# Kernel tuning notes

Measured on AMD Instinct MI355X. Metric: run time of the kernel, lower is better.

## Reference

```python
import jax, jax.numpy as jnp
import numpy as np

S, XD, C, R = 6, 3, 8, 64   # num_freqs, x_dim, num_channels, res_scale
N = 262144
STD = 0.001


def setup_inputs() -> dict:
    key = jax.random.key(0)
    k1, k2, k3 = jax.random.split(key, 3)
    x = jax.random.uniform(k1, (N, XD), dtype=jnp.float32)
    features = jax.random.normal(k2, (S, 2 * XD, C, R, R), dtype=jnp.float32) * STD
    features_2d = jax.random.normal(k3, (S, 2 * XD, C, R, R), dtype=jnp.float32) * STD
    return {"x": x, "features": features, "features_2d": features_2d}


def _bilinear(img, gx, gy):
    # img: [C,H,W]; gx,gy: [P] normalized coords in [-1,1]
    # bilinear grid_sample, align_corners=True, clamped (border) indices
    _, H, W = img.shape
    ix = (gx + 1.0) * 0.5 * (W - 1)
    iy = (gy + 1.0) * 0.5 * (H - 1)
    ix0f = jnp.floor(ix)
    iy0f = jnp.floor(iy)
    wx = ix - ix0f
    wy = iy - iy0f
    ix0 = jnp.clip(ix0f.astype(jnp.int32), 0, W - 1)
    iy0 = jnp.clip(iy0f.astype(jnp.int32), 0, H - 1)
    ix1 = jnp.clip(ix0 + 1, 0, W - 1)
    iy1 = jnp.clip(iy0 + 1, 0, H - 1)
    v00 = img[:, iy0, ix0]  # [C,P]
    v01 = img[:, iy0, ix1]
    v10 = img[:, iy1, ix0]
    v11 = img[:, iy1, ix1]
    return (v00 * (1 - wx) * (1 - wy) + v01 * wx * (1 - wy)
            + v10 * (1 - wx) * wy + v11 * wx * wy)


def reference(x, features, features_2d):
    n = x.shape[0]
    scales = 2.0 ** jnp.arange(S, dtype=x.dtype)                   # [S]
    xb = x[:, None, :] * scales[:, None]                           # [N,S,3]
    latent = jnp.sin(jnp.stack([xb, xb + 0.5 * jnp.pi], axis=-2))  # [N,S,2,3]

    B = S * 2 * XD  # 36 independent (scale, sin/cos, dim) lookups

    # 1D (line) lookup: grid x-coord fixed at 0, y-coord = encoded value
    gy = jnp.transpose(latent.reshape(n, S, 2 * XD), (1, 2, 0)).reshape(B, n)
    gx = jnp.zeros_like(gy)
    fs = jax.vmap(_bilinear)(features.reshape(B, C, R, R), gx, gy)  # [B,C,N]
    fs = fs.reshape(S, 2, XD, C, n)

    # 2D (plane) lookup with cyclic dim pairs (1,2),(2,0),(0,1)
    pairs = jnp.array([[1, 2], [2, 0], [0, 1]])
    g2 = latent[..., pairs]                                        # [N,S,2,3,2]
    gx2 = jnp.transpose(g2[..., 0], (1, 2, 3, 0)).reshape(B, n)
    gy2 = jnp.transpose(g2[..., 1], (1, 2, 3, 0)).reshape(B, n)
    fs2 = jax.vmap(_bilinear)(features_2d.reshape(B, C, R, R), gx2, gy2)
    fs2 = fs2.reshape(S, 2, XD, C, n)

    out = jnp.transpose(fs * fs2, (4, 3, 0, 1, 2))                 # [N,C,S,2,3]
    out = out + latent[:, None]                                    # + PE, broadcast over C
    return out.reshape(n, C * S * 2 * XD)                          # [N, 288]
```

## Files before the change

### kernel.cpp

```cpp
#include <hip/hip_runtime.h>

#define NS 6
#define NXD 3
#define NC 8
#define NR 64
#define NB 36
#define NPOINTS 262144
#define OUTD 288
#define PTS 32

__device__ __forceinline__ unsigned short f2bf(float f) {
    unsigned u = __float_as_uint(f);
    unsigned r = u + 0x7fffu + ((u >> 16) & 1u);
    return (unsigned short)(r >> 16);
}
__device__ __forceinline__ unsigned pack2(float a, float b) {
    return (unsigned)f2bf(a) | ((unsigned)f2bf(b) << 16);
}

#define QSCALE 8192.0f
#define QINV   (1.0f / 8192.0f)

__device__ __forceinline__ unsigned f2q8(float f) {
    float q = rintf(f * QSCALE);
    q = fminf(fmaxf(q, -127.0f), 127.0f);
    return (unsigned)((int)q) & 0xffu;
}

__global__ void build_pxq(const float* __restrict__ F2, unsigned* __restrict__ px) {
    int tid = blockIdx.x * 256 + threadIdx.x;
    const int total = NB * 64 * 64 * NC;
    if (tid >= total) return;
    int c  = tid & 7;
    int xx = (tid >> 3) & 63;
    int y  = (tid >> 9) & 63;
    int b  = tid >> 15;
    const float* img = F2 + (size_t)(b * NC + c) * (NR * NR);
    int x1 = xx < 63 ? xx + 1 : 63;
    int y1 = y  < 63 ? y  + 1 : 63;
    unsigned q00 = f2q8(img[y  * NR + xx]);
    unsigned q01 = f2q8(img[y  * NR + x1]);
    unsigned q10 = f2q8(img[y1 * NR + xx]);
    unsigned q11 = f2q8(img[y1 * NR + x1]);
    px[tid] = q00 | (q01 << 8) | (q10 << 16) | (q11 << 24);
}

__global__ void build_f1q(const float* __restrict__ F, unsigned* __restrict__ f1q) {
    int tid = blockIdx.x * 256 + threadIdx.x;
    const int total = NB * 64 * NC;
    if (tid >= total) return;
    int c = tid & 7;
    int y = (tid >> 3) & 63;
    int b = tid >> 9;
    const float* img = F + (size_t)(b * NC + c) * NR * NR;
    const float sc = 0.5f * QINV;
    float a = sc * (img[y * NR + 31] + img[y * NR + 32]);
    int y1 = y < 63 ? y + 1 : 63;
    float bb = sc * (img[y1 * NR + 31] + img[y1 * NR + 32]);
    f1q[tid] = pack2(a, bb);
}

__global__ __launch_bounds__(256, 4) void encode_kernel(
    const float* __restrict__ x,
    const unsigned* __restrict__ px,
    const unsigned* __restrict__ f1q,
    float* __restrict__ out)
{
    __shared__ float stage[PTS * 289];
    const int t = threadIdx.x;
    const int c = t & 7;
    const int u = t >> 3;
    const int n = blockIdx.x * PTS + u;

    const float xv0 = x[3 * n + 0];
    const float xv1 = x[3 * n + 1];
    const float xv2 = x[3 * n + 2];

    float* stg = &stage[u * 289];

    #pragma unroll
    for (int g = 0; g < 12; ++g) {
        const int s = g >> 1;
        const int p = g & 1;
        const float sc = (float)(1 << s);
        float l0, l1, l2;
        if (p == 0) {
            l0 = __sinf(xv0 * sc); l1 = __sinf(xv1 * sc); l2 = __sinf(xv2 * sc);
        } else {
            l0 = __cosf(xv0 * sc); l1 = __cosf(xv1 * sc); l2 = __cosf(xv2 * sc);
        }
        const int b0 = g * 3;
        #pragma unroll
        for (int k = 0; k < 3; ++k) {
            const int b = b0 + k;
            float gy1 = (k == 0) ? l0 : (k == 1) ? l1 : l2;
            float ga  = (k == 0) ? l1 : (k == 1) ? l2 : l0;
            float gb  = (k == 0) ? l2 : (k == 1) ? l0 : l1;

            float fy = fminf(fmaxf(__builtin_fmaf(gy1, 31.5f, 31.5f), 0.0f), 63.0f);
            float fy0 = floorf(fy);
            float wy = fy - fy0;
            int y0 = (int)fy0;
            unsigned pr = f1q[(b * 64 + y0) * 8 + c];
            float a0 = __uint_as_float(pr << 16);
            float a1 = __uint_as_float(pr & 0xffff0000u);
            float fsv = __builtin_fmaf(a1 - a0, wy, a0);

            float fx2 = fminf(fmaxf(__builtin_fmaf(ga, 31.5f, 31.5f), 0.0f), 63.0f);
            float fy2 = fminf(fmaxf(__builtin_fmaf(gb, 31.5f, 31.5f), 0.0f), 63.0f);
            float fx20 = floorf(fx2);
            float fy20 = floorf(fy2);
            float wx2 = fx2 - fx20;
            float wy2 = fy2 - fy20;
            int xx = (int)fx20;
            int yy = (int)fy20;
            unsigned w = px[((b * 64 + yy) * 64 + xx) * 8 + c];
            float v00 = (float)((int)(w << 24) >> 24);
            float v01 = (float)((int)(w << 16) >> 24);
            float v10 = (float)((int)(w <<  8) >> 24);
            float v11 = (float)((int)w        >> 24);
            float tp = __builtin_fmaf(v01 - v00, wx2, v00);
            float bt = __builtin_fmaf(v11 - v10, wx2, v10);
            float fs2v = __builtin_fmaf(bt - tp, wy2, tp);

            stg[c * 36 + b] = __builtin_fmaf(fsv, fs2v, gy1);
        }
    }
    __syncthreads();

    float* ob = out + (size_t)blockIdx.x * (PTS * OUTD);
    #pragma unroll
    for (int r = 0; r < 36; ++r) {
        int e = t + r * 256;
        int uu = e / 288;
        int v = e - uu * 288;
        ob[e] = stage[uu * 289 + v];
    }
}

extern "C" void kernel_launch(void* const* d_in, const int* in_sizes, int n_in,
                              void* d_out, int out_size, void* d_ws, size_t ws_size,
                              hipStream_t stream)
{
    const float* x  = (const float*)d_in[0];
    const float* F  = (const float*)d_in[1];
    const float* F2 = (const float*)d_in[2];
    float* out = (float*)d_out;

    unsigned* px  = (unsigned*)d_ws;
    unsigned* f1q = px + NB * 64 * 64 * NC;

    build_pxq<<<(NB * 64 * 64 * NC + 255) / 256, 256, 0, stream>>>(F2, px);
    build_f1q<<<(NB * 64 * NC + 255) / 256, 256, 0, stream>>>(F, f1q);
    encode_kernel<<<NPOINTS / PTS, 256, 0, stream>>>(x, px, f1q, out);
}
```

Before: 371.4 us.

## Split work per thread across scale halves and two channels with uint2 gathers

Reassigns each thread from one channel across all 36 lookups to two adjacent channels across half the scales (18 lookups). Table reads become 8-byte uint2 gathers, and the sin/cos and index math is shared between the two channels, halving transcendental and address work per output. The upper clamp to 63 is dropped because sin/cos outputs stay within range. The risk is more register pressure and a different bank pattern on the shared-memory stage writes.

```diff
diff --git a/kernel.cpp b/kernel.cpp
--- a/kernel.cpp
+++ b/kernel.cpp
@@ -67,63 +67,82 @@
     float* __restrict__ out)
 {
     __shared__ float stage[PTS * 289];
-    const int t = threadIdx.x;
-    const int c = t & 7;
-    const int u = t >> 3;
-    const int n = blockIdx.x * PTS + u;
+    const int t  = threadIdx.x;
+    const int c2 = t & 3;
+    const int h  = (t >> 2) & 1;
+    const int u  = t >> 3;
+    const int n  = blockIdx.x * PTS + u;
 
     const float xv0 = x[3 * n + 0];
     const float xv1 = x[3 * n + 1];
     const float xv2 = x[3 * n + 2];
 
-    float* stg = &stage[u * 289];
+    const float scb = h ? 8.0f : 1.0f;
+    const float a0v = xv0 * scb, a1v = xv1 * scb, a2v = xv2 * scb;
+
+    const int hb = 18 * h;
+    const unsigned* f1p = f1q + hb * 512 + 2 * c2;
+    const unsigned* pxp = px  + hb * 32768 + 2 * c2;
+    float* stg = &stage[u * 289 + (2 * c2) * 36];
 
     #pragma unroll
-    for (int g = 0; g < 12; ++g) {
-        const int s = g >> 1;
-        const int p = g & 1;
-        const float sc = (float)(1 << s);
+    for (int gg = 0; gg < 6; ++gg) {
+        const float m = (float)(1 << (gg >> 1));
         float l0, l1, l2;
-        if (p == 0) {
-            l0 = __sinf(xv0 * sc); l1 = __sinf(xv1 * sc); l2 = __sinf(xv2 * sc);
+        if ((gg & 1) == 0) {
+            l0 = __sinf(a0v * m); l1 = __sinf(a1v * m); l2 = __sinf(a2v * m);
         } else {
-            l0 = __cosf(xv0 * sc); l1 = __cosf(xv1 * sc); l2 = __cosf(xv2 * sc);
+            l0 = __cosf(a0v * m); l1 = __cosf(a1v * m); l2 = __cosf(a2v * m);
         }
-        const int b0 = g * 3;
         #pragma unroll
         for (int k = 0; k < 3; ++k) {
-            const int b = b0 + k;
+            const int bloc = 3 * gg + k;
             float gy1 = (k == 0) ? l0 : (k == 1) ? l1 : l2;
             float ga  = (k == 0) ? l1 : (k == 1) ? l2 : l0;
             float gb  = (k == 0) ? l2 : (k == 1) ? l0 : l1;
 
-            float fy = fminf(fmaxf(__builtin_fmaf(gy1, 31.5f, 31.5f), 0.0f), 63.0f);
+            float fy  = fmaxf(__builtin_fmaf(gy1, 31.5f, 31.5f), 0.0f);
             float fy0 = floorf(fy);
-            float wy = fy - fy0;
-            int y0 = (int)fy0;
-            unsigned pr = f1q[(b * 64 + y0) * 8 + c];
-            float a0 = __uint_as_float(pr << 16);
-            float a1 = __uint_as_float(pr & 0xffff0000u);
-            float fsv = __builtin_fmaf(a1 - a0, wy, a0);
+            float wy  = fy - fy0;
+            int   y0  = (int)fy0;
+            uint2 pr  = *(const uint2*)(f1p + bloc * 512 + y0 * 8);
 
-            float fx2 = fminf(fmaxf(__builtin_fmaf(ga, 31.5f, 31.5f), 0.0f), 63.0f);
-            float fy2 = fminf(fmaxf(__builtin_fmaf(gb, 31.5f, 31.5f), 0.0f), 63.0f);
+            float fx2  = fmaxf(__builtin_fmaf(ga, 31.5f, 31.5f), 0.0f);
+            float fy2  = fmaxf(__builtin_fmaf(gb, 31.5f, 31.5f), 0.0f);
             float fx20 = floorf(fx2);
             float fy20 = floorf(fy2);
-            float wx2 = fx2 - fx20;
-            float wy2 = fy2 - fy20;
-            int xx = (int)fx20;
-            int yy = (int)fy20;
-            unsigned w = px[((b * 64 + yy) * 64 + xx) * 8 + c];
-            float v00 = (float)((int)(w << 24) >> 24);
-            float v01 = (float)((int)(w << 16) >> 24);
-            float v10 = (float)((int)(w <<  8) >> 24);
-            float v11 = (float)((int)w        >> 24);
-            float tp = __builtin_fmaf(v01 - v00, wx2, v00);
-            float bt = __builtin_fmaf(v11 - v10, wx2, v10);
-            float fs2v = __builtin_fmaf(bt - tp, wy2, tp);
+            float wx2  = fx2 - fx20;
+            float wy2  = fy2 - fy20;
+            int   xx   = (int)fx20;
+            int   yy   = (int)fy20;
+            uint2 w    = *(const uint2*)(pxp + bloc * 32768 + yy * 512 + xx * 8);
 
-            stg[c * 36 + b] = __builtin_fmaf(fsv, fs2v, gy1);
+            {
+                float a0 = __uint_as_float(pr.x << 16);
+                float a1 = __uint_as_float(pr.x & 0xffff0000u);
+                float fsv = __builtin_fmaf(a1 - a0, wy, a0);
+                float v00 = (float)((int)(w.x << 24) >> 24);
+                float v01 = (float)((int)(w.x << 16) >> 24);
+                float v10 = (float)((int)(w.x <<  8) >> 24);
+                float v11 = (float)((int)w.x        >> 24);
+                float tp = __builtin_fmaf(v01 - v00, wx2, v00);
+                float bt = __builtin_fmaf(v11 - v10, wx2, v10);
+                float fs2v = __builtin_fmaf(bt - tp, wy2, tp);
+                stg[hb + bloc] = __builtin_fmaf(fsv, fs2v, gy1);
+            }
+            {
+                float a0 = __uint_as_float(pr.y << 16);
+                float a1 = __uint_as_float(pr.y & 0xffff0000u);
+                float fsv = __builtin_fmaf(a1 - a0, wy, a0);
+                float v00 = (float)((int)(w.y << 24) >> 24);
+                float v01 = (float)((int)(w.y << 16) >> 24);
+                float v10 = (float)((int)(w.y <<  8) >> 24);
+                float v11 = (float)((int)w.y        >> 24);
+                float tp = __builtin_fmaf(v01 - v00, wx2, v00);
+                float bt = __builtin_fmaf(v11 - v10, wx2, v10);
+                float fs2v = __builtin_fmaf(bt - tp, wy2, tp);
+                stg[36 + hb + bloc] = __builtin_fmaf(fsv, fs2v, gy1);
+            }
         }
     }
     __syncthreads();
```

Measured after the change: 370.9 us. No clear change (-0.1%).
